# Performance work log

Hardware: AMD Instinct MI355X
Metric: run time of the kernel (lower is better)

The kernel has to match this reference:

```python
import jax, jax.numpy as jnp
import numpy as np
from jax import lax

B, S_ENC, T, M = 32, 200, 400, 80
E2 = 512          # 2 * encoder_hidden_dim
H = 1024          # decoder_hidden_dim
IN0 = M + E2      # LSTM layer-0 input size


def setup_inputs() -> dict:
    key = jax.random.key(0)
    ks = jax.random.split(key, 16)
    s = 1.0 / np.sqrt(H)  # pytorch LSTM-style uniform scale ~ 1/sqrt(H)
    def rn(k, shape, scale):
        return jax.random.normal(k, shape, jnp.float32) * scale
    return {
        "encoder_outputs": rn(ks[0], (B, S_ENC, E2), 1.0),
        "audio_targets": rn(ks[1], (B, T, M), 1.0),
        "Wih0": rn(ks[2], (4 * H, IN0), s),
        "Whh0": rn(ks[3], (4 * H, H), s),
        "bih0": rn(ks[4], (4 * H,), s),
        "bhh0": rn(ks[5], (4 * H,), s),
        "Wih1": rn(ks[6], (4 * H, H), s),
        "Whh1": rn(ks[7], (4 * H, H), s),
        "bih1": rn(ks[8], (4 * H,), s),
        "bhh1": rn(ks[9], (4 * H,), s),
        "Wa": rn(ks[10], (1, H + E2), s),
        "ba": rn(ks[11], (1,), s),
        "Wfc": rn(ks[12], (M, H), s),
        "bfc": rn(ks[13], (M,), s),
        "audio_lengths": jax.random.randint(ks[14], (B,), 1, T + 1, dtype=jnp.int32),
    }


def _lstm_cell(x, h, c, Wih, Whh, b):
    # PyTorch gate order: i, f, g, o
    g = x @ Wih.T + h @ Whh.T + b
    i, f, gg, o = jnp.split(g, 4, axis=-1)
    c2 = jax.nn.sigmoid(f) * c + jax.nn.sigmoid(i) * jnp.tanh(gg)
    h2 = jax.nn.sigmoid(o) * jnp.tanh(c2)
    return h2, c2


def reference(encoder_outputs, audio_targets, Wih0, Whh0, bih0, bhh0,
              Wih1, Whh1, bih1, bhh1, Wa, ba, Wfc, bfc, audio_lengths):
    del audio_lengths  # unused in the original forward
    Hd = Whh0.shape[1]
    b0 = bih0 + bhh0
    b1 = bih1 + bhh1
    # tanh(concat(h, enc)) == concat(tanh(h), tanh(enc)) -> precompute enc part of the score once
    wa_h = Wa[0, :Hd]                 # [H]
    wa_e = Wa[0, Hd:]                 # [E2]
    enc_score = jnp.einsum('bse,e->bs', jnp.tanh(encoder_outputs), wa_e)  # [B,S]

    def step(carry, x_t):
        h0, c0, h1, c1 = carry
        score = enc_score + (jnp.tanh(h1) @ wa_h)[:, None] + ba[0]        # [B,S]
        w = jax.nn.softmax(score, axis=1)
        ctx = jnp.einsum('bs,bse->be', w, encoder_outputs)                # [B,E2]
        inp = jnp.concatenate([x_t, ctx], axis=-1)                        # [B,IN0]
        h0, c0 = _lstm_cell(inp, h0, c0, Wih0, Whh0, b0)
        h1, c1 = _lstm_cell(h0, h1, c1, Wih1, Whh1, b1)
        pred = h1 @ Wfc.T + bfc                                            # [B,M]
        return (h0, c0, h1, c1), pred

    bsz = encoder_outputs.shape[0]
    z = jnp.zeros((bsz, Hd), encoder_outputs.dtype)
    # t = 0: hidden is None -> context is mean over encoder steps, zero initial state
    ctx0 = encoder_outputs.mean(axis=1)
    inp0 = jnp.concatenate([audio_targets[:, 0, :], ctx0], axis=-1)
    h0, c0 = _lstm_cell(inp0, z, z, Wih0, Whh0, b0)
    h1, c1 = _lstm_cell(h0, z, z, Wih1, Whh1, b1)
    pred0 = h1 @ Wfc.T + bfc

    xs = jnp.swapaxes(audio_targets, 0, 1)[1:]                             # [T-1,B,M]
    _, preds = lax.scan(step, (h0, c0, h1, c1), xs)                        # [T-1,B,M]
    out = jnp.concatenate([pred0[:, None, :], jnp.swapaxes(preds, 0, 1)], axis=1)
    return out                                                             # [B,T,M]
```

## Files before the change

### kernel.cpp

```cpp
#include <hip/hip_runtime.h>
#include <hip/hip_cooperative_groups.h>

namespace cg = cooperative_groups;

#define BBAT 32
#define SE 200
#define TT 400
#define MM 80
#define EE 512
#define HH 1024
#define IN0 592
#define KS 608
#define NSC 19
#define W0S 1640
#define W1STR 1032
#define NBLK 256
#define NTHR 512

typedef __attribute__((ext_vector_type(4))) float f32x4;
typedef __attribute__((ext_vector_type(8))) short s16x8;
typedef unsigned long long u64;

#define OFF_W0    0
#define OFF_W1I   52480
#define OFF_W1H   85504
#define OFF_GRED  118528
#define OFF_C0    151296
#define OFF_C1    151808
#define OFF_BS    152320
#define LDS_TOTAL 152448

#define WS_XSTAT 0
#define WS_H0B   15564800
#define WS_H1B   15695872
#define WS_ESC   15892480
#define WS_CST   15918080
#define WS_FLG   16049152
#define H1OFFU   ((TT+1)*32*4)
#define FLGN     (2*(TT+1)*32*4)

__device__ __forceinline__ float sigmf(float x){ return 1.0f/(1.0f+expf(-x)); }

__device__ __forceinline__ unsigned short f2bf(float v){
  unsigned int u = __float_as_uint(v);
  u += 0x7fffu + ((u >> 16) & 1u);
  return (unsigned short)(u >> 16);
}
__device__ __forceinline__ float bf2f(unsigned short s){
  return __uint_as_float(((unsigned)s) << 16);
}

__device__ __forceinline__ void st64a(void* p, u64 v){
  __hip_atomic_store((u64*)p, v, __ATOMIC_RELAXED, __HIP_MEMORY_SCOPE_AGENT);
}
__device__ __forceinline__ u64 ld64a(const void* p){
  return __hip_atomic_load((const u64*)p, __ATOMIC_RELAXED, __HIP_MEMORY_SCOPE_AGENT);
}

#define LD4C(d0,d1,d2,d3,p0,p1,p2,p3) \
  asm volatile("global_load_dwordx4 %0, %4, off sc0 sc1\n\t" \
               "global_load_dwordx4 %1, %5, off sc0 sc1\n\t" \
               "global_load_dwordx4 %2, %6, off sc0 sc1\n\t" \
               "global_load_dwordx4 %3, %7, off sc0 sc1" \
               : "=&v"(d0), "=&v"(d1), "=&v"(d2), "=&v"(d3) \
               : "v"(p0), "v"(p1), "v"(p2), "v"(p3))

#define WAIT16(a0,a1,a2,a3,b0,b1,b2,b3,c0,c1,c2,c3,d0,d1,d2,d3) \
  asm volatile("s_waitcnt vmcnt(0)" \
    : "+v"(a0),"+v"(a1),"+v"(a2),"+v"(a3), \
      "+v"(b0),"+v"(b1),"+v"(b2),"+v"(b3), \
      "+v"(c0),"+v"(c1),"+v"(c2),"+v"(c3), \
      "+v"(d0),"+v"(d1),"+v"(d2),"+v"(d3))

__device__ __forceinline__ float bsum(float v, float* red){
  #pragma unroll
  for (int o = 32; o; o >>= 1) v += __shfl_down(v, o);
  __syncthreads();
  if ((threadIdx.x & 63) == 0) red[threadIdx.x >> 6] = v;
  __syncthreads();
  float s = 0.f;
  #pragma unroll
  for (int w2 = 0; w2 < 8; ++w2) s += red[w2];
  return s;
}
__device__ __forceinline__ float bmax(float v, float* red){
  #pragma unroll
  for (int o = 32; o; o >>= 1) v = fmaxf(v, __shfl_down(v, o));
  __syncthreads();
  if ((threadIdx.x & 63) == 0) red[threadIdx.x >> 6] = v;
  __syncthreads();
  float s = -3.4e38f;
  #pragma unroll
  for (int w2 = 0; w2 < 8; ++w2) s = fmaxf(s, red[w2]);
  return s;
}

#define MFMA16(a,b,c) __builtin_amdgcn_mfma_f32_16x16x32_bf16((a),(b),(c),0,0,0)

__device__ __forceinline__ void mfma_static(const unsigned short* __restrict__ xs,
    const unsigned short* __restrict__ W0, int w, int row, int kg,
    f32x4& acc0, f32x4& acc1)
{
  for (int c = w; c < NSC; c += 8) {
    const int off = (c << 5) + (kg << 3);
    s16x8 a0 = *(const s16x8*)(xs + (size_t)row*KS + off);
    s16x8 a1 = *(const s16x8*)(xs + (size_t)(row+16)*KS + off);
    s16x8 bw = *(const s16x8*)(W0 + row*W0S + off);
    acc0 = MFMA16(a0, bw, acc0);
    acc1 = MFMA16(a1, bw, acc1);
  }
}

__device__ __forceinline__ void fc_pair(const unsigned short* __restrict__ h1bF,
    const float* __restrict__ Wfc, const float* __restrict__ bfc,
    float* __restrict__ out, int b, int m, int tglob, int lane)
{
  const int c = lane >> 1, half = lane & 1;
  const unsigned short* hp = h1bF + (c << 10) + (b << 5) + (half << 4);
  const float* wp = Wfc + (size_t)m*HH + (c << 5) + (half << 4);
  float pp = 0.f;
  #pragma unroll
  for (int q4 = 0; q4 < 4; ++q4) {
    u64 hq = ld64a(hp + (q4 << 2));
    float4 wv = *(const float4*)(wp + (q4 << 2));
    pp = fmaf(bf2f((unsigned short)hq), wv.x,
         fmaf(bf2f((unsigned short)(hq >> 16)), wv.y,
         fmaf(bf2f((unsigned short)(hq >> 32)), wv.z,
         fmaf(bf2f((unsigned short)(hq >> 48)), wv.w, pp))));
  }
  #pragma unroll
  for (int o2 = 32; o2; o2 >>= 1) pp += __shfl_down(pp, o2);
  if (lane == 0) out[((size_t)b*TT + tglob)*MM + m] = pp + bfc[m];
}

__global__ void __launch_bounds__(NTHR, 1) decoder_kernel(
    const float* __restrict__ enc, const float* __restrict__ audio,
    const float* __restrict__ Wih0, const float* __restrict__ Whh0,
    const float* __restrict__ bih0, const float* __restrict__ bhh0,
    const float* __restrict__ Wih1, const float* __restrict__ Whh1,
    const float* __restrict__ bih1, const float* __restrict__ bhh1,
    const float* __restrict__ Wa, const float* __restrict__ ba,
    const float* __restrict__ Wfc, const float* __restrict__ bfc,
    float* __restrict__ out, float* __restrict__ ws)
{
  cg::grid_group grid = cg::this_grid();
  extern __shared__ char lds[];
  unsigned short* W0  = (unsigned short*)(lds + OFF_W0);
  unsigned short* W1I = (unsigned short*)(lds + OFF_W1I);
  unsigned short* W1H = (unsigned short*)(lds + OFF_W1H);
  float* Gred = (float*)(lds + OFF_GRED);
  float* c0l  = (float*)(lds + OFF_C0);
  float* c1l  = (float*)(lds + OFF_C1);
  float* b0s  = (float*)(lds + OFF_BS);
  float* b1s  = b0s + 16;
  float* smw  = Gred;
  float* red  = Gred + 256;

  const int blk = blockIdx.x, tid = threadIdx.x;
  const int j = blk;
  const int w = tid >> 6, lane = tid & 63;
  const int row = lane & 15, kg = lane >> 4;
  const int cblk = j >> 3;
  const int colw = (j & 7) << 2;
  const int eg = tid & 3, ep = (tid >> 2) & 3, eb = tid >> 4;

  unsigned short* xstat = (unsigned short*)((char*)ws + WS_XSTAT);
  unsigned short* h0b   = (unsigned short*)((char*)ws + WS_H0B);
  unsigned short* h1b   = (unsigned short*)((char*)ws + WS_H1B);
  float* esc  = (float*)((char*)ws + WS_ESC);
  float* cm   = (float*)((char*)ws + WS_CST);
  float* cs   = cm + BBAT*EE;
  unsigned* flg = (unsigned*)((char*)ws + WS_FLG);

  for (int i = tid; i < 16*W0S; i += NTHR) {
    int r = i / W0S, k = i - r*W0S;
    int n = (r & 3)*HH + 4*j + (r >> 2);
    float v = 0.f;
    if (k < IN0) v = Wih0[(size_t)n*IN0 + k];
    else if (k >= KS && k < KS + HH) v = Whh0[(size_t)n*HH + (k - KS)];
    W0[i] = f2bf(v);
  }
  for (int i = tid; i < 16*W1STR; i += NTHR) {
    int r = i / W1STR, k = i - r*W1STR;
    int n = (r & 3)*HH + 4*j + (r >> 2);
    W1I[i] = (k < HH) ? f2bf(Wih1[(size_t)n*HH + k]) : (unsigned short)0;
    W1H[i] = (k < HH) ? f2bf(Whh1[(size_t)n*HH + k]) : (unsigned short)0;
  }
  if (tid < 16) {
    int p = tid >> 2, g = tid & 3, n = g*HH + 4*j + p;
    b0s[tid] = bih0[n] + bhh0[n];
    b1s[tid] = bih1[n] + bhh1[n];
  }
  if (tid < 128) { c0l[tid] = 0.f; c1l[tid] = 0.f; }
  for (int i = blk*NTHR + tid; i < 2*BBAT*HH; i += NBLK*NTHR) h0b[i] = 0;
  for (int i = blk*NTHR + tid; i < 3*BBAT*HH; i += NBLK*NTHR) h1b[i] = 0;
  for (int i = blk*NTHR + tid; i < FLGN; i += NBLK*NTHR) flg[i] = 0u;
  for (int r2 = blk; r2 < BBAT*SE; r2 += NBLK) {
    float pp = tanhf(enc[(size_t)r2*EE + tid]) * Wa[HH + tid];
    pp = bsum(pp, red);
    if (tid == 0) esc[r2] = pp;
  }
  grid.sync();

  if (blk < BBAT) {
    const int b = blk;
    float sc = (tid < SE) ? esc[b*SE + tid] : -3.4e38f;
    float mx = bmax(sc, red);
    float ex = (tid < SE) ? expf(sc - mx) : 0.f;
    float den = bsum(ex, red);
    if (tid < SE) smw[tid] = ex / den;
    __syncthreads();
    const int e = tid;
    float as = 0.f, am = 0.f;
    for (int s = 0; s < SE; ++s) {
      float v = enc[((size_t)b*SE + s)*EE + e];
      as = fmaf(smw[s], v, as);
      am += v;
    }
    cm[b*EE + e] = am * (1.0f/(float)SE);
    cs[b*EE + e] = as;
  }
  grid.sync();

  for (int t2 = blk; t2 < TT; t2 += NBLK) {
    const float* cx = (t2 == 0) ? cm : cs;
    for (int b = 0; b < BBAT; ++b) {
      for (int k = tid; k < KS; k += NTHR) {
        float v;
        if (k < MM)        v = audio[((size_t)b*TT + t2)*MM + k];
        else if (k < IN0)  v = cx[b*EE + (k - MM)];
        else               v = 0.f;
        xstat[((size_t)t2*BBAT + b)*KS + k] = f2bf(v);
      }
    }
  }
  grid.sync();

  const f32x4 z4 = {0.f,0.f,0.f,0.f};
  f32x4 accP0 = z4, accP1 = z4;

  mfma_static(xstat, W0, w, row, kg, accP0, accP1);
  {
    float* gw = Gred + (w << 10) + row;
    #pragma unroll
    for (int v = 0; v < 4; ++v) {
      gw[(((kg<<2)+v)    << 4)] = accP0[v];
      gw[(((kg<<2)+v+16) << 4)] = accP1[v];
    }
    __syncthreads();
    float s0 = 0.f;
    #pragma unroll
    for (int w8 = 0; w8 < 8; ++w8) s0 += Gred[(w8 << 10) + tid];
    float ga = s0;
    float gb = __shfl_xor(s0, 1);
    float gc = __shfl_xor(s0, 2);
    float gd = __shfl_xor(gb, 2);
    if (eg == 0) {
      f32x4 bi = *(const f32x4*)(b0s + (ep << 2));
      float gi = ga + bi[0], gg = gc + bi[2], go = gd + bi[3];
      float cn = sigmf(gi) * tanhf(gg);
      c0l[ep*32 + eb] = cn;
      float hn = sigmf(go) * tanhf(cn);
      float hB = __shfl_xor(hn, 4);
      float hC = __shfl_xor(hn, 8);
      float hD = __shfl_xor(hB, 8);
      if ((tid & 15) == 0) {
        u64 hp = (u64)f2bf(hn) | ((u64)f2bf(hB) << 16) | ((u64)f2bf(hC) << 32) | ((u64)f2bf(hD) << 48);
        st64a(h0b + (cblk << 10) + (eb << 5) + colw, hp);
      }
    }
  }
  __builtin_amdgcn_s_waitcnt(0);
  __syncthreads();
  if (tid == 0)
    __hip_atomic_fetch_add(flg + (size_t)cblk*4, 1u, __ATOMIC_RELAXED, __HIP_MEMORY_SCOPE_AGENT);
  accP0 = z4; accP1 = z4;
  mfma_static(xstat + (size_t)BBAT*KS, W0, w, row, kg, accP0, accP1);

  int s1w = 0;
  for (int t = 0; t < TT; ++t) {
    const int s1r = (s1w == 0) ? 2 : s1w - 1;
    const unsigned short* h0R = h0b + (t&1)*BBAT*HH;
    const unsigned short* h1R = h1b + (size_t)s1r*BBAT*HH;
    unsigned short* h1W = h1b + (size_t)s1w*BBAT*HH;
    unsigned short* h0Wn = h0b + ((t+1)&1)*BBAT*HH;

    {
      const int pc = w + ((lane & 3) << 3);
      if (lane < 4) {
        unsigned* fp = flg + ((size_t)t*32 + pc)*4;
        while (__hip_atomic_load(fp, __ATOMIC_RELAXED, __HIP_MEMORY_SCOPE_AGENT) < 8u)
          __builtin_amdgcn_s_sleep(1);
      } else if (lane < 8 && t > 0) {
        unsigned* fp = flg + H1OFFU + ((size_t)(t-1)*32 + pc)*4;
        while (__hip_atomic_load(fp, __ATOMIC_RELAXED, __HIP_MEMORY_SCOPE_AGENT) < 8u)
          __builtin_amdgcn_s_sleep(1);
      }
      asm volatile("" ::: "memory");
    }

    s16x8 A0h[4], A1h[4], A0g[4], A1g[4];
    {
      const unsigned short* ph0a  = h0R + (row << 5) + (kg << 3);
      const unsigned short* ph0b_ = h0R + ((row+16) << 5) + (kg << 3);
      const unsigned short* ph1a  = h1R + (row << 5) + (kg << 3);
      const unsigned short* ph1b_ = h1R + ((row+16) << 5) + (kg << 3);
      const int o0 = (w << 10), o1 = ((w+8) << 10), o2_ = ((w+16) << 10), o3 = ((w+24) << 10);
      LD4C(A0h[0],A0h[1],A0h[2],A0h[3], ph0a+o0, ph0a+o1, ph0a+o2_, ph0a+o3);
      LD4C(A1h[0],A1h[1],A1h[2],A1h[3], ph0b_+o0, ph0b_+o1, ph0b_+o2_, ph0b_+o3);
      LD4C(A0g[0],A0g[1],A0g[2],A0g[3], ph1a+o0, ph1a+o1, ph1a+o2_, ph1a+o3);
      LD4C(A1g[0],A1g[1],A1g[2],A1g[3], ph1b_+o0, ph1b_+o1, ph1b_+o2_, ph1b_+o3);
      WAIT16(A0h[0],A0h[1],A0h[2],A0h[3], A1h[0],A1h[1],A1h[2],A1h[3],
             A0g[0],A0g[1],A0g[2],A0g[3], A1g[0],A1g[1],A1g[2],A1g[3]);
    }
    f32x4 q0 = z4, q1 = z4;
    #pragma unroll
    for (int i = 0; i < 4; ++i) {
      const int off = ((w + (i << 3)) << 5) + (kg << 3);
      s16x8 b1 = *(const s16x8*)(W1I + row*W1STR + off);
      q0 = MFMA16(A0h[i], b1, q0);
      q1 = MFMA16(A1h[i], b1, q1);
      s16x8 b0 = *(const s16x8*)(W0 + row*W0S + KS + off);
      accP0 = MFMA16(A0h[i], b0, accP0);
      accP1 = MFMA16(A1h[i], b0, accP1);
      s16x8 b2 = *(const s16x8*)(W1H + row*W1STR + off);
      q0 = MFMA16(A0g[i], b2, q0);
      q1 = MFMA16(A1g[i], b2, q1);
    }
    {
      float* gw = Gred + (w << 10) + row;
      #pragma unroll
      for (int v = 0; v < 4; ++v) {
        gw[(((kg<<2)+v)    << 4)]       = accP0[v];
        gw[(((kg<<2)+v+16) << 4)]       = accP1[v];
        gw[512 + (((kg<<2)+v)    << 4)] = q0[v];
        gw[512 + (((kg<<2)+v+16) << 4)] = q1[v];
      }
      __syncthreads();
      float s0 = 0.f, s1 = 0.f;
      #pragma unroll
      for (int w8 = 0; w8 < 8; ++w8) {
        s0 += Gred[(w8 << 10) + tid];
        s1 += Gred[(w8 << 10) + 512 + tid];
      }
      float a0g_ = s0;
      float b0g_ = __shfl_xor(s0, 1);
      float c0g_ = __shfl_xor(s0, 2);
      float d0g_ = __shfl_xor(b0g_, 2);
      float a1g_ = s1;
      float b1g_ = __shfl_xor(s1, 1);
      float c1g_ = __shfl_xor(s1, 2);
      float d1g_ = __shfl_xor(b1g_, 2);
      if (eg == 0) {
        f32x4 bi1 = *(const f32x4*)(b1s + (ep << 2));
        float gi = a1g_ + bi1[0], gf = b1g_ + bi1[1], gg = c1g_ + bi1[2], go = d1g_ + bi1[3];
        float cn1 = sigmf(gf) * c1l[ep*32 + eb] + sigmf(gi) * tanhf(gg);
        c1l[ep*32 + eb] = cn1;
        float hn1 = sigmf(go) * tanhf(cn1);
        f32x4 bi0 = *(const f32x4*)(b0s + (ep << 2));
        float fi = a0g_ + bi0[0], ff = b0g_ + bi0[1], fg = c0g_ + bi0[2], fo = d0g_ + bi0[3];
        float cn0 = sigmf(ff) * c0l[ep*32 + eb] + sigmf(fi) * tanhf(fg);
        c0l[ep*32 + eb] = cn0;
        float hn0 = sigmf(fo) * tanhf(cn0);
        float h1B = __shfl_xor(hn1, 4);
        float h1C = __shfl_xor(hn1, 8);
        float h1D = __shfl_xor(h1B, 8);
        float h0B = __shfl_xor(hn0, 4);
        float h0C = __shfl_xor(hn0, 8);
        float h0D = __shfl_xor(h0B, 8);
        if ((tid & 15) == 0) {
          u64 hp1 = (u64)f2bf(hn1) | ((u64)f2bf(h1B) << 16) | ((u64)f2bf(h1C) << 32) | ((u64)f2bf(h1D) << 48);
          st64a(h1W + (cblk << 10) + (eb << 5) + colw, hp1);
          u64 hp0 = (u64)f2bf(hn0) | ((u64)f2bf(h0B) << 16) | ((u64)f2bf(h0C) << 32) | ((u64)f2bf(h0D) << 48);
          st64a(h0Wn + (cblk << 10) + (eb << 5) + colw, hp0);
        }
      }
    }
    __builtin_amdgcn_s_waitcnt(0);
    __syncthreads();
    if (tid == 0) {
      __hip_atomic_fetch_add(flg + ((size_t)(t+1)*32 + cblk)*4, 1u, __ATOMIC_RELAXED, __HIP_MEMORY_SCOPE_AGENT);
      __hip_atomic_fetch_add(flg + H1OFFU + ((size_t)t*32 + cblk)*4, 1u, __ATOMIC_RELAXED, __HIP_MEMORY_SCOPE_AGENT);
    }

    if (t >= 1) {
      const unsigned short* h1bF = h1b + (size_t)s1r*BBAT*HH;
      for (int u = w; u < 10; u += 8) {
        int idx = j*10 + u;
        int b = idx / MM, m = idx - b*MM;
        fc_pair(h1bF, Wfc, bfc, out, b, m, t-1, lane);
      }
    }
    accP0 = z4; accP1 = z4;
    if (t + 2 < TT)
      mfma_static(xstat + (size_t)(t+2)*BBAT*KS, W0, w, row, kg, accP0, accP1);
    s1w = (s1w == 2) ? 0 : s1w + 1;
  }

  if (tid < 32) {
    unsigned* fp = flg + H1OFFU + ((size_t)(TT-1)*32 + tid)*4;
    while (__hip_atomic_load(fp, __ATOMIC_RELAXED, __HIP_MEMORY_SCOPE_AGENT) < 8u)
      __builtin_amdgcn_s_sleep(1);
  }
  __syncthreads();
  {
    const unsigned short* h1bF = h1b + (size_t)((TT-1) % 3)*BBAT*HH;
    for (int u = w; u < 10; u += 8) {
      int idx = j*10 + u;
      int b = idx / MM, m = idx - b*MM;
      fc_pair(h1bF, Wfc, bfc, out, b, m, TT-1, lane);
    }
  }
}

extern "C" void kernel_launch(void* const* d_in, const int* in_sizes, int n_in,
                              void* d_out, int out_size, void* d_ws, size_t ws_size,
                              hipStream_t stream) {
  const float* enc  = (const float*)d_in[0];
  const float* audio= (const float*)d_in[1];
  const float* Wih0 = (const float*)d_in[2];
  const float* Whh0 = (const float*)d_in[3];
  const float* bih0 = (const float*)d_in[4];
  const float* bhh0 = (const float*)d_in[5];
  const float* Wih1 = (const float*)d_in[6];
  const float* Whh1 = (const float*)d_in[7];
  const float* bih1 = (const float*)d_in[8];
  const float* bhh1 = (const float*)d_in[9];
  const float* Wa   = (const float*)d_in[10];
  const float* ba   = (const float*)d_in[11];
  const float* Wfc  = (const float*)d_in[12];
  const float* bfc  = (const float*)d_in[13];
  float* out = (float*)d_out;
  float* ws  = (float*)d_ws;

  (void)hipFuncSetAttribute((const void*)decoder_kernel,
                            hipFuncAttributeMaxDynamicSharedMemorySize, LDS_TOTAL);

  void* args[] = { &enc,&audio,&Wih0,&Whh0,&bih0,&bhh0,&Wih1,&Whh1,&bih1,&bhh1,
                   &Wa,&ba,&Wfc,&bfc,&out,&ws };
  hipLaunchCooperativeKernel((const void*)decoder_kernel, dim3(NBLK), dim3(NTHR),
                             args, LDS_TOTAL, stream);
}
```

Before: 2.927 ms.

## Defer output projection to a post-loop phase using full h1 history

The triple-buffered h1 ring is replaced by a buffer holding the h1 state of every timestep. The per-step FC projection is removed from the recurrent loop, and all 400 timesteps are projected after a grid sync, parallelised across blocks. This takes the FC loads and reductions off the serial critical path of each step. The cost is a much larger workspace (about 26 MB of h1 history) and an extra output phase after the loop.

```diff
diff --git a/kernel.cpp b/kernel.cpp
--- a/kernel.cpp
+++ b/kernel.cpp
@@ -32,10 +32,10 @@
 
 #define WS_XSTAT 0
 #define WS_H0B   15564800
-#define WS_H1B   15695872
-#define WS_ESC   15892480
-#define WS_CST   15918080
-#define WS_FLG   16049152
+#define WS_H1H   15695872
+#define WS_ESC   41975808
+#define WS_CST   42001408
+#define WS_FLG   42132480
 #define H1OFFU   ((TT+1)*32*4)
 #define FLGN     (2*(TT+1)*32*4)
 
@@ -52,9 +52,6 @@
 
 __device__ __forceinline__ void st64a(void* p, u64 v){
   __hip_atomic_store((u64*)p, v, __ATOMIC_RELAXED, __HIP_MEMORY_SCOPE_AGENT);
-}
-__device__ __forceinline__ u64 ld64a(const void* p){
-  return __hip_atomic_load((const u64*)p, __ATOMIC_RELAXED, __HIP_MEMORY_SCOPE_AGENT);
 }
 
 #define LD4C(d0,d1,d2,d3,p0,p1,p2,p3) \
@@ -109,28 +106,6 @@
     acc0 = MFMA16(a0, bw, acc0);
     acc1 = MFMA16(a1, bw, acc1);
   }
-}
-
-__device__ __forceinline__ void fc_pair(const unsigned short* __restrict__ h1bF,
-    const float* __restrict__ Wfc, const float* __restrict__ bfc,
-    float* __restrict__ out, int b, int m, int tglob, int lane)
-{
-  const int c = lane >> 1, half = lane & 1;
-  const unsigned short* hp = h1bF + (c << 10) + (b << 5) + (half << 4);
-  const float* wp = Wfc + (size_t)m*HH + (c << 5) + (half << 4);
-  float pp = 0.f;
-  #pragma unroll
-  for (int q4 = 0; q4 < 4; ++q4) {
-    u64 hq = ld64a(hp + (q4 << 2));
-    float4 wv = *(const float4*)(wp + (q4 << 2));
-    pp = fmaf(bf2f((unsigned short)hq), wv.x,
-         fmaf(bf2f((unsigned short)(hq >> 16)), wv.y,
-         fmaf(bf2f((unsigned short)(hq >> 32)), wv.z,
-         fmaf(bf2f((unsigned short)(hq >> 48)), wv.w, pp))));
-  }
-  #pragma unroll
-  for (int o2 = 32; o2; o2 >>= 1) pp += __shfl_down(pp, o2);
-  if (lane == 0) out[((size_t)b*TT + tglob)*MM + m] = pp + bfc[m];
 }
 
 __global__ void __launch_bounds__(NTHR, 1) decoder_kernel(
@@ -166,7 +141,7 @@
 
   unsigned short* xstat = (unsigned short*)((char*)ws + WS_XSTAT);
   unsigned short* h0b   = (unsigned short*)((char*)ws + WS_H0B);
-  unsigned short* h1b   = (unsigned short*)((char*)ws + WS_H1B);
+  unsigned short* h1h   = (unsigned short*)((char*)ws + WS_H1H);
   float* esc  = (float*)((char*)ws + WS_ESC);
   float* cm   = (float*)((char*)ws + WS_CST);
   float* cs   = cm + BBAT*EE;
@@ -193,7 +168,7 @@
   }
   if (tid < 128) { c0l[tid] = 0.f; c1l[tid] = 0.f; }
   for (int i = blk*NTHR + tid; i < 2*BBAT*HH; i += NBLK*NTHR) h0b[i] = 0;
-  for (int i = blk*NTHR + tid; i < 3*BBAT*HH; i += NBLK*NTHR) h1b[i] = 0;
+  for (int i = blk*NTHR + tid; i < BBAT*HH; i += NBLK*NTHR) h1h[i] = 0;
   for (int i = blk*NTHR + tid; i < FLGN; i += NBLK*NTHR) flg[i] = 0u;
   for (int r2 = blk; r2 < BBAT*SE; r2 += NBLK) {
     float pp = tanhf(enc[(size_t)r2*EE + tid]) * Wa[HH + tid];
@@ -258,6 +233,7 @@
     if (eg == 0) {
       f32x4 bi = *(const f32x4*)(b0s + (ep << 2));
       float gi = ga + bi[0], gg = gc + bi[2], go = gd + bi[3];
+      (void)gb;
       float cn = sigmf(gi) * tanhf(gg);
       c0l[ep*32 + eb] = cn;
       float hn = sigmf(go) * tanhf(cn);
@@ -277,12 +253,10 @@
   accP0 = z4; accP1 = z4;
   mfma_static(xstat + (size_t)BBAT*KS, W0, w, row, kg, accP0, accP1);
 
-  int s1w = 0;
   for (int t = 0; t < TT; ++t) {
-    const int s1r = (s1w == 0) ? 2 : s1w - 1;
     const unsigned short* h0R = h0b + (t&1)*BBAT*HH;
-    const unsigned short* h1R = h1b + (size_t)s1r*BBAT*HH;
-    unsigned short* h1W = h1b + (size_t)s1w*BBAT*HH;
+    const unsigned short* h1R = h1h + (size_t)t*BBAT*HH;
+    unsigned short* h1W = h1h + (size_t)(t+1)*BBAT*HH;
     unsigned short* h0Wn = h0b + ((t+1)&1)*BBAT*HH;
 
     {
@@ -383,32 +357,40 @@
       __hip_atomic_fetch_add(flg + H1OFFU + ((size_t)t*32 + cblk)*4, 1u, __ATOMIC_RELAXED, __HIP_MEMORY_SCOPE_AGENT);
     }
 
-    if (t >= 1) {
-      const unsigned short* h1bF = h1b + (size_t)s1r*BBAT*HH;
-      for (int u = w; u < 10; u += 8) {
-        int idx = j*10 + u;
-        int b = idx / MM, m = idx - b*MM;
-        fc_pair(h1bF, Wfc, bfc, out, b, m, t-1, lane);
-      }
-    }
     accP0 = z4; accP1 = z4;
     if (t + 2 < TT)
       mfma_static(xstat + (size_t)(t+2)*BBAT*KS, W0, w, row, kg, accP0, accP1);
-    s1w = (s1w == 2) ? 0 : s1w + 1;
-  }
-
-  if (tid < 32) {
-    unsigned* fp = flg + H1OFFU + ((size_t)(TT-1)*32 + tid)*4;
-    while (__hip_atomic_load(fp, __ATOMIC_RELAXED, __HIP_MEMORY_SCOPE_AGENT) < 8u)
-      __builtin_amdgcn_s_sleep(1);
-  }
-  __syncthreads();
+  }
+
+  grid.sync();
   {
-    const unsigned short* h1bF = h1b + (size_t)((TT-1) % 3)*BBAT*HH;
-    for (int u = w; u < 10; u += 8) {
-      int idx = j*10 + u;
-      int b = idx / MM, m = idx - b*MM;
-      fc_pair(h1bF, Wfc, bfc, out, b, m, TT-1, lane);
+    const int g2 = tid >> 3, l = tid & 7;
+    for (int tt = blk; tt < TT; tt += NBLK) {
+      const unsigned short* hh = h1h + (size_t)(tt+1)*BBAT*HH;
+      for (int pass = 0; pass < 40; ++pass) {
+        const int idx = pass*64 + g2;
+        const int b = idx / MM, m = idx - b*MM;
+        float pp = 0.f;
+        #pragma unroll
+        for (int ci = 0; ci < 4; ++ci) {
+          const int c = (l << 2) + ci;
+          const unsigned short* hp = hh + (c << 10) + (b << 5);
+          const float* wp = Wfc + (size_t)m*HH + (c << 5);
+          #pragma unroll
+          for (int q = 0; q < 8; ++q) {
+            u64 hq = *(const u64*)(hp + (q << 2));
+            float4 wv = *(const float4*)(wp + (q << 2));
+            pp = fmaf(bf2f((unsigned short)hq), wv.x,
+                 fmaf(bf2f((unsigned short)(hq >> 16)), wv.y,
+                 fmaf(bf2f((unsigned short)(hq >> 32)), wv.z,
+                 fmaf(bf2f((unsigned short)(hq >> 48)), wv.w, pp))));
+          }
+        }
+        pp += __shfl_down(pp, 4);
+        pp += __shfl_down(pp, 2);
+        pp += __shfl_down(pp, 1);
+        if (l == 0) out[((size_t)b*TT + tt)*MM + m] = pp + bfc[m];
+      }
     }
   }
 }
```

New measurement: 3.271 ms. +11.8%, slower.
